# Optimization experiments

Hardware: AMD Instinct MI355X
Metric: run time of the kernel (lower is better)

Reference implementation:

```python
import jax, jax.numpy as jnp
import numpy as np

B, C, H, W = 8, 256, 64, 64
D = C // 8  # qk proj dim = 32
R = C // 8  # channel-SE reduction dim = 32

def setup_inputs() -> dict:
    key = jax.random.key(0)
    ks = jax.random.split(key, 10)
    s = lambda *sh: 1.0 / np.sqrt(sh[-1])
    return {
        'x':  jax.random.normal(ks[0], (B, C, H, W), jnp.float32),
        'Wq': jax.random.normal(ks[1], (D, C), jnp.float32) * s(D, C),
        'bq': jnp.zeros((D,), jnp.float32),
        'Wk': jax.random.normal(ks[2], (D, C), jnp.float32) * s(D, C),
        'bk': jnp.zeros((D,), jnp.float32),
        'Wv': jax.random.normal(ks[3], (C, C), jnp.float32) * s(C, C),
        'bv': jnp.zeros((C,), jnp.float32),
        'gamma': jnp.ones((1,), jnp.float32),
        'W1': jax.random.normal(ks[4], (R, 2 * C), jnp.float32) * s(R, 2 * C),
        'W2': jax.random.normal(ks[5], (C, R), jnp.float32) * s(C, R),
        'lamb': jnp.ones((1,), jnp.float32),
    }

def reference(x, Wq, bq, Wk, bk, Wv, bv, gamma, W1, W2, lamb):
    b, c, h, w = x.shape
    n = h * w
    xf = x.reshape(b, c, n)  # [B,C,N]
    # --- spatial self-attention (1x1 convs == matmuls over channel dim) ---
    q = jnp.einsum('dc,bcn->bnd', Wq, xf) + bq            # [B,N,D]
    k = jnp.einsum('dc,bcn->bdn', Wk, xf) + bk[:, None]   # [B,D,N]
    attn = jax.nn.softmax(jnp.einsum('bnd,bdm->bnm', q, k), axis=-1)  # [B,N,N]
    v = jnp.einsum('dc,bcn->bdn', Wv, xf) + bv[:, None]   # [B,C,N]
    # out[b,c,m] = sum_n v[b,c,n] * attn[b,m,n]  (torch: bmm(v, attn^T))
    sp = jnp.einsum('bcn,bmn->bcm', v, attn).reshape(b, c, h, w)
    sp = gamma * sp
    # --- channel SE-gate ---
    mean = jnp.mean(xf, axis=-1)                # [B,C]
    std = jnp.std(xf, axis=-1, ddof=1)          # torch.std uses unbiased (ddof=1)
    inp = jnp.concatenate([mean, std], axis=1)  # [B,2C]
    a = jax.nn.sigmoid(jax.nn.relu(inp @ W1.T) @ W2.T)  # [B,C]
    ch = lamb * a[:, :, None, None] * x
    return sp + ch + x
```

## Files before the change

### kernel.cpp

```cpp
#include <hip/hip_runtime.h>
#include <hip/hip_bf16.h>

#define Bb 8
#define Cc 256
#define Nn 4096
#define Dd 32

typedef short bf16x8 __attribute__((ext_vector_type(8)));
typedef short bf16x4 __attribute__((ext_vector_type(4)));
typedef float f32x4 __attribute__((ext_vector_type(4)));

__device__ __forceinline__ void glds16(const void* g, void* l) {
    __builtin_amdgcn_global_load_lds(
        (const __attribute__((address_space(1))) unsigned int*)g,
        (__attribute__((address_space(3))) unsigned int*)l, 16, 0, 0);
}

__global__ __launch_bounds__(256) void convt_kernel(
    const float* __restrict__ x, __hip_bfloat16* __restrict__ x_t,
    float* __restrict__ sum_ws, float* __restrict__ sumsq_ws)
{
    __shared__ __hip_bfloat16 tile[64][68];
    const int n0 = blockIdx.x * 64, c0 = blockIdx.y * 64, b = blockIdx.z;
    const int t = threadIdx.x;

#pragma unroll
    for (int i = 0; i < 4; i++) {
        int id = i * 256 + t;
        int row = id >> 4, col4 = id & 15;
        float4 v = *(const float4*)(x + ((size_t)(b * Cc + c0 + row)) * Nn + n0 + col4 * 4);
        bf16x4 bv;
        bv[0] = __bfloat16_as_short(__float2bfloat16(v.x));
        bv[1] = __bfloat16_as_short(__float2bfloat16(v.y));
        bv[2] = __bfloat16_as_short(__float2bfloat16(v.z));
        bv[3] = __bfloat16_as_short(__float2bfloat16(v.w));
        *(bf16x4*)((void*)&tile[row][col4 * 4]) = bv;
        float ls  = v.x + v.y + v.z + v.w;
        float ls2 = v.x * v.x + v.y * v.y + v.z * v.z + v.w * v.w;
        ls  += __shfl_xor(ls, 1, 16);  ls2 += __shfl_xor(ls2, 1, 16);
        ls  += __shfl_xor(ls, 2, 16);  ls2 += __shfl_xor(ls2, 2, 16);
        ls  += __shfl_xor(ls, 4, 16);  ls2 += __shfl_xor(ls2, 4, 16);
        ls  += __shfl_xor(ls, 8, 16);  ls2 += __shfl_xor(ls2, 8, 16);
        if ((t & 15) == 0) {
            atomicAdd(&sum_ws[b * Cc + c0 + row], ls);
            atomicAdd(&sumsq_ws[b * Cc + c0 + row], ls2);
        }
    }
    __syncthreads();
#pragma unroll
    for (int i = 0; i < 2; i++) {
        int id = i * 256 + t;
        int nl = id >> 3, cg = id & 7;
        bf16x8 o;
#pragma unroll
        for (int j = 0; j < 8; j++) o[j] = __bfloat16_as_short(tile[cg * 8 + j][nl]);
        *(bf16x8*)(x_t + ((size_t)(b * Nn + n0 + nl)) * Cc + c0 + cg * 8) = o;
    }
}

__global__ __launch_bounds__(256) void wconv_kernel(
    const float* __restrict__ Wq, const float* __restrict__ Wk, const float* __restrict__ Wv,
    __hip_bfloat16* __restrict__ w_bf)
{
    const int ct = blockIdx.x;
    const int t = threadIdx.x;
#pragma unroll
    for (int i = 0; i < 8; i++) {
        int g = i * 256 + t;
        int row = g >> 5, c8 = g & 31;
        int c0 = c8 * 8;
        int grow = ct * 64 + row;
        const float* src;
        if (grow < 32)       src = Wq + (size_t)grow * Cc + c0;
        else if (grow < 64)  src = Wk + (size_t)(grow - 32) * Cc + c0;
        else                 src = Wv + (size_t)(grow - 64) * Cc + c0;
        float4 v0 = *(const float4*)src;
        float4 v1 = *(const float4*)(src + 4);
        bf16x8 o;
        o[0] = __bfloat16_as_short(__float2bfloat16(v0.x));
        o[1] = __bfloat16_as_short(__float2bfloat16(v0.y));
        o[2] = __bfloat16_as_short(__float2bfloat16(v0.z));
        o[3] = __bfloat16_as_short(__float2bfloat16(v0.w));
        o[4] = __bfloat16_as_short(__float2bfloat16(v1.x));
        o[5] = __bfloat16_as_short(__float2bfloat16(v1.y));
        o[6] = __bfloat16_as_short(__float2bfloat16(v1.z));
        o[7] = __bfloat16_as_short(__float2bfloat16(v1.w));
        int kchunk = c0 >> 5, qd = (c0 & 31) >> 3, cg = row >> 4, rl = row & 15;
        *(bf16x8*)(w_bf + ((size_t)ct * 32 + kchunk * 4 + cg) * 512 + (qd * 16 + rl) * 8) = o;
    }
}

__global__ __launch_bounds__(256, 2) void proj_kernel(
    const __hip_bfloat16* __restrict__ x_t, const __hip_bfloat16* __restrict__ w_bf,
    const float* __restrict__ bq, const float* __restrict__ bk, const float* __restrict__ bv,
    __hip_bfloat16* __restrict__ q_ws, __hip_bfloat16* __restrict__ k_ws,
    __hip_bfloat16* __restrict__ v_ws)
{
    __shared__ __hip_bfloat16 ldsX[32 * 512];
    __shared__ __hip_bfloat16 ldsW[32 * 512];

    const int n0 = blockIdx.x * 64;
    const int ct = blockIdx.y;
    const int b  = blockIdx.z;
    const int t = threadIdx.x;
    const int w = t >> 6, lane = t & 63, quad = lane >> 4, l15 = lane & 15;

#pragma unroll
    for (int j = 0; j < 8; j++) {
        int idx = w * 8 + j;
        int kchunk = idx >> 2, ngrp = idx & 3;
        glds16(x_t + ((size_t)(b * Nn + n0 + ngrp * 16 + l15)) * Cc + kchunk * 32 + quad * 8,
               ldsX + idx * 512);
        glds16(w_bf + ((size_t)ct * 32 + idx) * 512 + lane * 8, ldsW + idx * 512);
    }
    __syncthreads();

    f32x4 acc[4];
#pragma unroll
    for (int cg = 0; cg < 4; cg++) {
        int gcol = ct * 64 + cg * 16 + l15;
        float bias = (gcol < 32) ? bq[gcol] : (gcol < 64 ? bk[gcol - 32] : bv[gcol - 64]);
        acc[cg] = (f32x4){bias, bias, bias, bias};
    }

#pragma unroll
    for (int kchunk = 0; kchunk < 8; kchunk++) {
        bf16x8 a = *(const bf16x8*)(ldsX + ((kchunk * 4 + w) * 64 + lane) * 8);
#pragma unroll
        for (int cg = 0; cg < 4; cg++) {
            bf16x8 bw = *(const bf16x8*)(ldsW + ((kchunk * 4 + cg) * 64 + lane) * 8);
            acc[cg] = __builtin_amdgcn_mfma_f32_16x16x32_bf16(a, bw, acc[cg], 0, 0, 0);
        }
    }

#pragma unroll
    for (int cg = 0; cg < 4; cg++) {
        int gcol = ct * 64 + cg * 16 + l15;
        int nb = n0 + w * 16 + quad * 4;
        if (gcol < 64) {
            __hip_bfloat16* dst = (gcol < 32) ? q_ws : k_ws;
            int d = gcol & 31;
#pragma unroll
            for (int r = 0; r < 4; r++)
                dst[((size_t)(b * Nn + nb + r)) * Dd + d] = __float2bfloat16(acc[cg][r]);
        } else {
            int c = gcol - 64;
            bf16x4 o;
#pragma unroll
            for (int r = 0; r < 4; r++) o[r] = __bfloat16_as_short(__float2bfloat16(acc[cg][r]));
            *(bf16x4*)(v_ws + ((size_t)(b * Cc + c)) * Nn + nb) = o;
        }
    }
}

__global__ __launch_bounds__(256) void gate_kernel(
    const float* __restrict__ sum_ws, const float* __restrict__ sumsq_ws,
    const float* __restrict__ W1, const float* __restrict__ W2,
    const float* __restrict__ lamb, float* __restrict__ coef)
{
    int b = blockIdx.x;
    __shared__ float inp[2 * Cc];
    __shared__ float h[32];
    int t = threadIdx.x;
    float s  = sum_ws[b * Cc + t];
    float s2 = sumsq_ws[b * Cc + t];
    float m   = s / Nn;
    float var = (s2 - (float)Nn * m * m) / (float)(Nn - 1);
    inp[t]      = m;
    inp[Cc + t] = sqrtf(fmaxf(var, 0.f));
    __syncthreads();
    if (t < 32) {
        float a = 0.f;
        for (int i = 0; i < 2 * Cc; i++) a += W1[t * (2 * Cc) + i] * inp[i];
        h[t] = fmaxf(a, 0.f);
    }
    __syncthreads();
    float g = 0.f;
#pragma unroll
    for (int r = 0; r < 32; r++) g += W2[t * 32 + r] * h[r];
    float a = 1.f / (1.f + __expf(-g));
    coef[b * Cc + t] = 1.f + lamb[0] * a;
}

__global__ __launch_bounds__(512, 2) void attn_kernel(
    const __hip_bfloat16* __restrict__ q_ws, const __hip_bfloat16* __restrict__ k_ws,
    const __hip_bfloat16* __restrict__ v_ws, const float* __restrict__ coef,
    const float* __restrict__ x, const float* __restrict__ gamma_p,
    float* __restrict__ out)
{
    extern __shared__ __hip_bfloat16 smem[];
    __hip_bfloat16* vbuf0 = smem;
    __hip_bfloat16* vbuf1 = smem + 16384;
    __hip_bfloat16* kbuf0 = smem + 32768;
    __hip_bfloat16* kbuf1 = smem + 36864;
    __hip_bfloat16* pbuf0 = smem + 40960;
    __hip_bfloat16* pbuf1 = smem + 49152;

    const int b  = blockIdx.x & 7;
    const int m0 = (blockIdx.x >> 3) * 128;
    const int t = threadIdx.x;
    const int w = t >> 6, lane = t & 63, quad = lane >> 4, l15 = lane & 15;
    const int mf0 = (w >> 1) * 2, chalf = w & 1;

    const bf16x8 aq = *(const bf16x8*)(q_ws + ((size_t)(b * Nn + m0 + w * 16 + l15)) * Dd + quad * 8);

    const __hip_bfloat16* vsrc[4];
#pragma unroll
    for (int j = 0; j < 4; j++) {
        int idx = w * 4 + j;
        int ch = idx >> 4, tc = idx & 15;
        vsrc[j] = v_ws + ((size_t)(b * Cc + tc * 16 + l15)) * Nn + ch * 32 + quad * 8;
    }
    const __hip_bfloat16* ksrc = k_ws + ((size_t)(b * Nn + w * 16 + l15)) * Dd + quad * 8;

#pragma unroll
    for (int j = 0; j < 4; j++) glds16(vsrc[j], vbuf0 + (w * 4 + j) * 512);
    glds16(ksrc, kbuf0 + w * 512);
    __syncthreads();

    f32x4 acc[2][8];
#pragma unroll
    for (int i = 0; i < 2; i++)
#pragma unroll
        for (int j = 0; j < 8; j++) acc[i][j] = (f32x4){0.f, 0.f, 0.f, 0.f};
    f32x4 accl[2] = {(f32x4){0.f,0.f,0.f,0.f}, (f32x4){0.f,0.f,0.f,0.f}};

    bf16x8 ones;
#pragma unroll
    for (int i = 0; i < 8; i++) ones[i] = (short)0x3F80;

    for (int it = 0; it < Nn / 64; it++) {
        const __hip_bfloat16* kb = (((it >> 1) & 1) ? kbuf1 : kbuf0) + (it & 1) * 2048;
        f32x4 s[4];
#pragma unroll
        for (int tt = 0; tt < 4; tt++) {
            bf16x8 bk = *(const bf16x8*)(kb + (tt * 64 + lane) * 8);
            s[tt] = __builtin_amdgcn_mfma_f32_16x16x32_bf16(aq, bk, (f32x4){0.f,0.f,0.f,0.f}, 0, 0, 0);
        }
        __hip_bfloat16* pb = (it & 1) ? pbuf1 : pbuf0;
#pragma unroll
        for (int tt = 0; tt < 4; tt++) {
            int nn = (tt & 1) * 16 + l15;
            __hip_bfloat16* pd = pb + (w * 2 + (tt >> 1)) * 512
                               + ((nn >> 3) * 16 + quad * 4) * 8 + (nn & 7);
#pragma unroll
            for (int r = 0; r < 4; r++)
                pd[r * 8] = __float2bfloat16(__expf(s[tt][r]));
        }

        __syncthreads();

        if (it + 1 < Nn / 64) {
            __hip_bfloat16* vn = ((it + 1) & 1) ? vbuf1 : vbuf0;
#pragma unroll
            for (int j = 0; j < 4; j++)
                glds16(vsrc[j] + (size_t)(it + 1) * 64, vn + (w * 4 + j) * 512);
        }
        if ((it & 1) == 0 && it + 2 < Nn / 64) {
            int sl = (it >> 1) + 1;
            glds16(ksrc + (size_t)(sl * 128) * Dd, ((sl & 1) ? kbuf1 : kbuf0) + w * 512);
        }

        const __hip_bfloat16* vb = (it & 1) ? vbuf1 : vbuf0;
        const __hip_bfloat16* pr = pb;
#pragma unroll
        for (int kc = 0; kc < 2; kc++) {
            bf16x8 ap0 = *(const bf16x8*)(pr + (((mf0    ) * 2 + kc) * 64 + lane) * 8);
            bf16x8 ap1 = *(const bf16x8*)(pr + (((mf0 + 1) * 2 + kc) * 64 + lane) * 8);
            accl[0] = __builtin_amdgcn_mfma_f32_16x16x32_bf16(ap0, ones, accl[0], 0, 0, 0);
            accl[1] = __builtin_amdgcn_mfma_f32_16x16x32_bf16(ap1, ones, accl[1], 0, 0, 0);
#pragma unroll
            for (int tcl = 0; tcl < 8; tcl++) {
                bf16x8 bv = *(const bf16x8*)(vb + ((kc * 16 + chalf * 8 + tcl) * 64 + lane) * 8);
                acc[0][tcl] = __builtin_amdgcn_mfma_f32_16x16x32_bf16(ap0, bv, acc[0][tcl], 0, 0, 0);
                acc[1][tcl] = __builtin_amdgcn_mfma_f32_16x16x32_bf16(ap1, bv, acc[1][tcl], 0, 0, 0);
            }
        }
    }

    const float g = gamma_p[0];
    float inv[2][4];
#pragma unroll
    for (int mfi = 0; mfi < 2; mfi++)
#pragma unroll
        for (int r = 0; r < 4; r++) inv[mfi][r] = g / accl[mfi][r];

#pragma unroll
    for (int mfi = 0; mfi < 2; mfi++) {
#pragma unroll
        for (int tcl = 0; tcl < 8; tcl++) {
            int c = (chalf * 8 + tcl) * 16 + l15;
            float cf = coef[b * Cc + c];
            size_t base = ((size_t)(b * Cc + c)) * Nn + m0 + (mf0 + mfi) * 16 + quad * 4;
#pragma unroll
            for (int r = 0; r < 4; r++)
                out[base + r] = acc[mfi][tcl][r] * inv[mfi][r] + cf * x[base + r];
        }
    }
}

extern "C" void kernel_launch(void* const* d_in, const int* in_sizes, int n_in,
                              void* d_out, int out_size, void* d_ws, size_t ws_size,
                              hipStream_t stream) {
    const float* x     = (const float*)d_in[0];
    const float* Wq    = (const float*)d_in[1];
    const float* bq    = (const float*)d_in[2];
    const float* Wk    = (const float*)d_in[3];
    const float* bk    = (const float*)d_in[4];
    const float* Wv    = (const float*)d_in[5];
    const float* bv    = (const float*)d_in[6];
    const float* gamma = (const float*)d_in[7];
    const float* W1    = (const float*)d_in[8];
    const float* W2    = (const float*)d_in[9];
    const float* lamb  = (const float*)d_in[10];
    float* out = (float*)d_out;

    char* ws = (char*)d_ws;
    __hip_bfloat16* q_ws = (__hip_bfloat16*)ws;
    __hip_bfloat16* k_ws = (__hip_bfloat16*)(ws + (2u  << 20));
    __hip_bfloat16* v_ws = (__hip_bfloat16*)(ws + (4u  << 20));
    __hip_bfloat16* x_t  = (__hip_bfloat16*)(ws + (20u << 20));
    float* sum_ws   = (float*)(ws + (36u << 20));
    float* sumsq_ws = sum_ws + Bb * Cc;
    float* coef     = sumsq_ws + Bb * Cc;
    __hip_bfloat16* w_bf = (__hip_bfloat16*)(ws + (37u << 20));

    (void)hipFuncSetAttribute((const void*)attn_kernel,
                              hipFuncAttributeMaxDynamicSharedMemorySize, 114688);

    hipMemsetAsync(sum_ws, 0, 2 * Bb * Cc * sizeof(float), stream);
    wconv_kernel<<<5, 256, 0, stream>>>(Wq, Wk, Wv, w_bf);
    convt_kernel<<<dim3(Nn / 64, Cc / 64, Bb), 256, 0, stream>>>(x, x_t, sum_ws, sumsq_ws);
    proj_kernel<<<dim3(Nn / 64, 5, Bb), 256, 0, stream>>>(x_t, w_bf, bq, bk, bv, q_ws, k_ws, v_ws);
    gate_kernel<<<Bb, 256, 0, stream>>>(sum_ws, sumsq_ws, W1, W2, lamb, coef);
    attn_kernel<<<256, 512, 114688, stream>>>(q_ws, k_ws, v_ws, coef, x, gamma, out);
}
```

Measured before the change: 244.4 us.

## Retile attention PV warps to 4x4 MFMA tiles and share row sums via LDS

```diff
diff --git a/kernel.cpp b/kernel.cpp
--- a/kernel.cpp
+++ b/kernel.cpp
@@ -99,9 +99,10 @@
     __shared__ __hip_bfloat16 ldsX[32 * 512];
     __shared__ __hip_bfloat16 ldsW[32 * 512];
 
-    const int n0 = blockIdx.x * 64;
-    const int ct = blockIdx.y;
-    const int b  = blockIdx.z;
+    const int b   = blockIdx.x & 7;
+    const int id2 = blockIdx.x >> 3;
+    const int ct  = id2 >> 6;
+    const int n0  = (id2 & 63) * 64;
     const int t = threadIdx.x;
     const int w = t >> 6, lane = t & 63, quad = lane >> 4, l15 = lane & 15;
 
@@ -200,7 +201,8 @@
     const int m0 = (blockIdx.x >> 3) * 128;
     const int t = threadIdx.x;
     const int w = t >> 6, lane = t & 63, quad = lane >> 4, l15 = lane & 15;
-    const int mf0 = (w >> 1) * 2, chalf = w & 1;
+    const int mf0 = (w >> 2) * 4;
+    const int tc0 = (w & 3) * 4;
 
     const bf16x8 aq = *(const bf16x8*)(q_ws + ((size_t)(b * Nn + m0 + w * 16 + l15)) * Dd + quad * 8);
 
@@ -218,12 +220,12 @@
     glds16(ksrc, kbuf0 + w * 512);
     __syncthreads();
 
-    f32x4 acc[2][8];
-#pragma unroll
-    for (int i = 0; i < 2; i++)
-#pragma unroll
-        for (int j = 0; j < 8; j++) acc[i][j] = (f32x4){0.f, 0.f, 0.f, 0.f};
-    f32x4 accl[2] = {(f32x4){0.f,0.f,0.f,0.f}, (f32x4){0.f,0.f,0.f,0.f}};
+    f32x4 acc[4][4];
+#pragma unroll
+    for (int i = 0; i < 4; i++)
+#pragma unroll
+        for (int j = 0; j < 4; j++) acc[i][j] = (f32x4){0.f, 0.f, 0.f, 0.f};
+    f32x4 accl = (f32x4){0.f, 0.f, 0.f, 0.f};
 
     bf16x8 ones;
 #pragma unroll
@@ -265,36 +267,48 @@
         const __hip_bfloat16* pr = pb;
 #pragma unroll
         for (int kc = 0; kc < 2; kc++) {
-            bf16x8 ap0 = *(const bf16x8*)(pr + (((mf0    ) * 2 + kc) * 64 + lane) * 8);
-            bf16x8 ap1 = *(const bf16x8*)(pr + (((mf0 + 1) * 2 + kc) * 64 + lane) * 8);
-            accl[0] = __builtin_amdgcn_mfma_f32_16x16x32_bf16(ap0, ones, accl[0], 0, 0, 0);
-            accl[1] = __builtin_amdgcn_mfma_f32_16x16x32_bf16(ap1, ones, accl[1], 0, 0, 0);
-#pragma unroll
-            for (int tcl = 0; tcl < 8; tcl++) {
-                bf16x8 bv = *(const bf16x8*)(vb + ((kc * 16 + chalf * 8 + tcl) * 64 + lane) * 8);
-                acc[0][tcl] = __builtin_amdgcn_mfma_f32_16x16x32_bf16(ap0, bv, acc[0][tcl], 0, 0, 0);
-                acc[1][tcl] = __builtin_amdgcn_mfma_f32_16x16x32_bf16(ap1, bv, acc[1][tcl], 0, 0, 0);
+            bf16x8 ap[4];
+#pragma unroll
+            for (int i = 0; i < 4; i++)
+                ap[i] = *(const bf16x8*)(pr + (((mf0 + i) * 2 + kc) * 64 + lane) * 8);
+            accl = __builtin_amdgcn_mfma_f32_16x16x32_bf16(ap[w & 3], ones, accl, 0, 0, 0);
+#pragma unroll
+            for (int tcl = 0; tcl < 4; tcl++) {
+                bf16x8 bv = *(const bf16x8*)(vb + ((kc * 16 + tc0 + tcl) * 64 + lane) * 8);
+#pragma unroll
+                for (int i = 0; i < 4; i++)
+                    acc[i][tcl] = __builtin_amdgcn_mfma_f32_16x16x32_bf16(ap[i], bv, acc[i][tcl], 0, 0, 0);
             }
         }
     }
 
+    float* ldsL = (float*)smem;
+    __syncthreads();
+    if (l15 == 0) {
+#pragma unroll
+        for (int r = 0; r < 4; r++) ldsL[w * 16 + quad * 4 + r] = accl[r];
+    }
+    __syncthreads();
+
     const float g = gamma_p[0];
-    float inv[2][4];
-#pragma unroll
-    for (int mfi = 0; mfi < 2; mfi++)
-#pragma unroll
-        for (int r = 0; r < 4; r++) inv[mfi][r] = g / accl[mfi][r];
-
-#pragma unroll
-    for (int mfi = 0; mfi < 2; mfi++) {
-#pragma unroll
-        for (int tcl = 0; tcl < 8; tcl++) {
-            int c = (chalf * 8 + tcl) * 16 + l15;
+    f32x4 inv[4];
+#pragma unroll
+    for (int i = 0; i < 4; i++) {
+        f32x4 lr = *(const f32x4*)(ldsL + (mf0 + i) * 16 + quad * 4);
+#pragma unroll
+        for (int r = 0; r < 4; r++) inv[i][r] = g / lr[r];
+    }
+
+#pragma unroll
+    for (int i = 0; i < 4; i++) {
+#pragma unroll
+        for (int tcl = 0; tcl < 4; tcl++) {
+            int c = (tc0 + tcl) * 16 + l15;
             float cf = coef[b * Cc + c];
-            size_t base = ((size_t)(b * Cc + c)) * Nn + m0 + (mf0 + mfi) * 16 + quad * 4;
+            size_t base = ((size_t)(b * Cc + c)) * Nn + m0 + (mf0 + i) * 16 + quad * 4;
 #pragma unroll
             for (int r = 0; r < 4; r++)
-                out[base + r] = acc[mfi][tcl][r] * inv[mfi][r] + cf * x[base + r];
+                out[base + r] = acc[i][tcl][r] * inv[i][r] + cf * x[base + r];
         }
     }
 }
@@ -331,7 +345,7 @@
     hipMemsetAsync(sum_ws, 0, 2 * Bb * Cc * sizeof(float), stream);
     wconv_kernel<<<5, 256, 0, stream>>>(Wq, Wk, Wv, w_bf);
     convt_kernel<<<dim3(Nn / 64, Cc / 64, Bb), 256, 0, stream>>>(x, x_t, sum_ws, sumsq_ws);
-    proj_kernel<<<dim3(Nn / 64, 5, Bb), 256, 0, stream>>>(x_t, w_bf, bq, bk, bv, q_ws, k_ws, v_ws);
+    proj_kernel<<<Bb * 5 * (Nn / 64), 256, 0, stream>>>(x_t, w_bf, bq, bk, bv, q_ws, k_ws, v_ws);
     gate_kernel<<<Bb, 256, 0, stream>>>(sum_ws, sumsq_ws, W1, W2, lamb, coef);
     attn_kernel<<<256, 512, 114688, stream>>>(q_ws, k_ws, v_ws, coef, x, gamma, out);
 }
```

Measured after the change: 601.0 us. 146% more time.
